# Kernel tuning notes

Measured on AMD Instinct MI355X. Metric: run time of the kernel, lower is better.

Reference implementation:

```python
import jax, jax.numpy as jnp
import numpy as np

DIM = 256
NUM_HEADS = 4
HEAD_DIM = DIM // NUM_HEADS


def setup_inputs() -> dict:
    key = jax.random.key(0)
    ks = jax.random.split(key, 8)
    B, N, C = 4, 2048, DIM
    x = jax.random.normal(ks[0], (B, N, C), dtype=jnp.float32)
    R = jax.random.normal(ks[1], (B, 3, 3), dtype=jnp.float32)
    P = jax.random.normal(ks[2], (N, 3), dtype=jnp.float32)
    s = 1.0 / np.sqrt(C)
    qkv_w = jax.random.normal(ks[3], (3 * C, C), dtype=jnp.float32) * s
    qkv_b = jax.random.normal(ks[4], (3 * C,), dtype=jnp.float32) * 0.02
    proj_w = jax.random.normal(ks[5], (C, C), dtype=jnp.float32) * s
    proj_b = jax.random.normal(ks[6], (C,), dtype=jnp.float32) * 0.02
    pos_scale = jnp.asarray(1.0, dtype=jnp.float32)
    return {"x": x, "R": R, "P": P, "qkv_w": qkv_w, "qkv_b": qkv_b,
            "proj_w": proj_w, "proj_b": proj_b, "pos_scale": pos_scale}


def reference(x, R, P, qkv_w, qkv_b, proj_w, proj_b, pos_scale):
    B, N, C = x.shape
    H, D = NUM_HEADS, HEAD_DIM
    scale = D ** -0.5
    # qkv: (B,N,3C) -> (3,B,H,N,D)
    qkv = (x @ qkv_w.T + qkv_b).reshape(B, N, 3, H, D).transpose(2, 0, 3, 1, 4)
    q, k, v = qkv[0], qkv[1], qkv[2]
    # attention logits (B,H,N,N)
    attn = jnp.einsum('bhid,bhjd->bhij', q, k) * scale
    # positional bias: RP = (R @ P^T)^T -> (B,N,3); bias_ij = dot(RP_i, P_j)
    RP = jnp.einsum('bab,jb->bja', R, P) if False else jnp.einsum('bca,ja->bjc', jnp.swapaxes(R, 1, 2), P)
    RP = jnp.einsum('bcd,jd->bjc', R, P)  # (B,N,3): (R @ P.T).T
    bias = jnp.einsum('bik,jk->bij', RP, P)[:, None, :, :] * pos_scale  # (B,1,N,N) broadcast over heads
    attn = jax.nn.softmax(attn + bias, axis=-1)
    out = jnp.einsum('bhij,bhjd->bhid', attn, v)  # (B,H,N,D)
    out = out.transpose(0, 2, 1, 3).reshape(B, N, C)
    out = out @ proj_w.T + proj_b
    return out
```

## Files before the change

kernel.cpp:

```cpp
#include <hip/hip_runtime.h>
#include <hip/hip_bf16.h>

#define B_ 4
#define N_ 2048
#define C_ 256
#define H_ 4
#define D_ 64

typedef __attribute__((ext_vector_type(8))) short bf16x8;
typedef __attribute__((ext_vector_type(4))) float f32x4;

#define LOG2E 1.4426950408889634f

static __device__ inline unsigned short f2bf(float f) {
    unsigned u = __builtin_bit_cast(unsigned, f);
    unsigned r = (u + 0x7fffu + ((u >> 16) & 1u)) >> 16;
    return (unsigned short)r;
}
static __device__ inline float bf2f(unsigned short h) {
    unsigned u = ((unsigned)h) << 16;
    return __builtin_bit_cast(float, u);
}
static __device__ inline unsigned pack2(float a, float b) {
    __hip_bfloat162 h = __float22bfloat162_rn(make_float2(a, b));
    unsigned u;
    __builtin_memcpy(&u, &h, 4);
    return u;
}
static __device__ inline bf16x8 ld_frag(const unsigned short* p) {
    return __builtin_bit_cast(bf16x8, *(const uint4*)p);
}
static __device__ inline void gload_lds16(const unsigned short* g, unsigned short* l) {
    __builtin_amdgcn_global_load_lds(
        (const __attribute__((address_space(1))) unsigned int*)(g),
        (__attribute__((address_space(3))) unsigned int*)(l),
        16, 0, 0);
}

__global__ __launch_bounds__(256) void cvt_kernel(
    const float* __restrict__ x, const float* __restrict__ qkv_w,
    const float* __restrict__ proj_w, const float* __restrict__ Pm,
    unsigned short* __restrict__ xb, unsigned short* __restrict__ wqb,
    unsigned short* __restrict__ wpb, unsigned short* __restrict__ eb)
{
    const int bid = blockIdx.x, tid = threadIdx.x;
    if (bid >= 1152) {
        const int n = (bid - 1152) * 256 + tid;
        const float* pp = Pm + n * 3;
        float p0 = pp[0], p1 = pp[1], p2 = pp[2];
        unsigned u0 = f2bf(p0), u1 = f2bf(p1), u2 = f2bf(p2);
        unsigned v0 = f2bf(p0 - bf2f((unsigned short)u0));
        unsigned v1 = f2bf(p1 - bf2f((unsigned short)u1));
        unsigned v2 = f2bf(p2 - bf2f((unsigned short)u2));
        uint4 lo, hi;
        lo.x = u0 | (u1 << 16); lo.y = u2 | (v0 << 16);
        lo.z = v1 | (v2 << 16); lo.w = u0 | (u1 << 16);
        hi.x = u2; hi.y = 0u; hi.z = 0u; hi.w = 0u;
        *(uint4*)&eb[n * 16 + 0] = lo;
        *(uint4*)&eb[n * 16 + 8] = hi;
        return;
    }
    const float* s; unsigned short* d; int i;
    if (bid < 1024)      { s = x;      d = xb;  i = (bid * 256 + tid) * 8; }
    else if (bid < 1120) { s = qkv_w;  d = wqb; i = ((bid - 1024) * 256 + tid) * 8; }
    else                 { s = proj_w; d = wpb; i = ((bid - 1120) * 256 + tid) * 8; }
    float4 a = *(const float4*)(s + i);
    float4 b = *(const float4*)(s + i + 4);
    uint4 u;
    u.x = pack2(a.x, a.y); u.y = pack2(a.z, a.w);
    u.z = pack2(b.x, b.y); u.w = pack2(b.z, b.w);
    *(uint4*)(d + i) = u;
}

__global__ __launch_bounds__(256) void qkv_gemm(
    const unsigned short* __restrict__ xb, const unsigned short* __restrict__ wb,
    const float* __restrict__ bias, unsigned short* __restrict__ qb,
    unsigned short* __restrict__ kb, unsigned short* __restrict__ vt)
{
    __shared__ __align__(16) unsigned short As[128 * 40];
    __shared__ __align__(16) unsigned short Bs[128 * 40];
    const int m0 = blockIdx.x * 128, o0 = blockIdx.y * 128;
    const int tid = threadIdx.x;
    const int wave = tid >> 6, lane = tid & 63, quad = lane >> 4, l16 = lane & 15;
    const int wy = wave >> 1, wx = wave & 1;

    f32x4 acc[4][4];
    #pragma unroll
    for (int i = 0; i < 4; ++i)
        #pragma unroll
        for (int j = 0; j < 4; ++j) acc[i][j] = (f32x4){0.f, 0.f, 0.f, 0.f};

    const int srow = tid >> 1, soff = (tid & 1) * 16;

    for (int k0 = 0; k0 < 256; k0 += 32) {
        __syncthreads();
        {
            const unsigned short* sa = &xb[(size_t)(m0 + srow) * 256 + k0 + soff];
            const unsigned short* sb = &wb[(size_t)(o0 + srow) * 256 + k0 + soff];
            *(uint4*)&As[srow * 40 + soff + 0] = *(const uint4*)(sa + 0);
            *(uint4*)&As[srow * 40 + soff + 8] = *(const uint4*)(sa + 8);
            *(uint4*)&Bs[srow * 40 + soff + 0] = *(const uint4*)(sb + 0);
            *(uint4*)&Bs[srow * 40 + soff + 8] = *(const uint4*)(sb + 8);
        }
        __syncthreads();
        bf16x8 a[4], b[4];
        #pragma unroll
        for (int mt = 0; mt < 4; ++mt) a[mt] = ld_frag(&As[(wy * 64 + mt * 16 + l16) * 40 + quad * 8]);
        #pragma unroll
        for (int nt = 0; nt < 4; ++nt) b[nt] = ld_frag(&Bs[(wx * 64 + nt * 16 + l16) * 40 + quad * 8]);
        #pragma unroll
        for (int mt = 0; mt < 4; ++mt)
            #pragma unroll
            for (int nt = 0; nt < 4; ++nt)
                acc[mt][nt] = __builtin_amdgcn_mfma_f32_16x16x32_bf16(a[mt], b[nt], acc[mt][nt], 0, 0, 0);
    }

    const int sec = o0 + wx * 64;
    const int three = sec >> 8;
    const int h = (sec >> 6) & 3;
    const int b = m0 >> 11;
    float bv[4];
    #pragma unroll
    for (int nt = 0; nt < 4; ++nt) bv[nt] = bias[sec + nt * 16 + l16];

    if (three == 2) {
        const int n64 = (m0 + wy * 64) & 2047;
        const size_t bh64 = ((size_t)b * H_ + h) * 64;
        #pragma unroll
        for (int nt = 0; nt < 4; ++nt) {
            int d = nt * 16 + l16;
            #pragma unroll
            for (int r = 0; r < 4; ++r) {
                ushort4 v;
                v.x = f2bf(acc[0][nt][r] + bv[nt]);
                v.y = f2bf(acc[1][nt][r] + bv[nt]);
                v.z = f2bf(acc[2][nt][r] + bv[nt]);
                v.w = f2bf(acc[3][nt][r] + bv[nt]);
                *(ushort4*)&vt[(bh64 + d) * N_ + n64 + 16 * quad + 4 * r] = v;
            }
        }
    } else {
        unsigned short* dst = (three == 0) ? qb : kb;
        float sc = (three == 0) ? (0.125f * LOG2E) : 1.0f;
        #pragma unroll
        for (int mt = 0; mt < 4; ++mt)
            #pragma unroll
            for (int r = 0; r < 4; ++r) {
                int n = (m0 + wy * 64 + mt * 16 + quad * 4 + r) & 2047;
                size_t rowbase = (((size_t)b * H_ + h) * N_ + n) * D_;
                #pragma unroll
                for (int nt = 0; nt < 4; ++nt)
                    dst[rowbase + nt * 16 + l16] = f2bf((acc[mt][nt][r] + bv[nt]) * sc);
            }
    }
}

#define LDK 64

__global__ __launch_bounds__(256) void attn_kernel(
    const unsigned short* __restrict__ qb, const unsigned short* __restrict__ kb,
    const unsigned short* __restrict__ vt, const unsigned short* __restrict__ eb,
    const float* __restrict__ Rm, const float* __restrict__ Pm,
    const float* __restrict__ ps_ptr,
    unsigned short* __restrict__ Opart, float* __restrict__ ml)
{
    __shared__ __align__(16) unsigned short Ks[2][64 * LDK];
    __shared__ __align__(16) unsigned short Vs[2][64 * LDK];
    __shared__ __align__(16) unsigned short Ps[64 * LDK];

    const int bh = blockIdx.y;
    const int b = bh >> 2;
    const int i0 = blockIdx.x * 64;
    const int split = blockIdx.z;
    const int tid = threadIdx.x;
    const int wave = tid >> 6, lane = tid & 63;
    const int quad = lane >> 4, l16 = lane & 15;
    const int x7 = l16 & 7;
    const float ps = ps_ptr[0];

    const size_t base = (size_t)bh * N_ * D_;
    const unsigned short* qg = qb + base;
    const unsigned short* kg = kb + base;
    const unsigned short* vg = vt + base;

    const int jbeg = split * (N_ / 2);
    const int NT = (N_ / 2) / 64;

    const int rl = lane >> 3, sl = lane & 7;
    const int swz = (sl ^ rl) * 8;
    const unsigned short* kq = kg + (size_t)(jbeg + wave * 16 + rl) * D_ + swz;
    const unsigned short* vq = vg + (size_t)(wave * 16 + rl) * N_ + jbeg + swz;
    const unsigned short* ep = eb + (size_t)(jbeg + l16) * 16 + (quad & 1) * 8;

    auto ISSUE = [&](int nb) {
        unsigned short* kd = &Ks[nb][(wave * 16) * LDK];
        unsigned short* vd = &Vs[nb][(wave * 16) * LDK];
        gload_lds16(kq,           kd);
        gload_lds16(kq + 8 * D_,  kd + 8 * LDK);
        gload_lds16(vq,           vd);
        gload_lds16(vq + 8 * N_,  vd + 8 * LDK);
    };

    ISSUE(0);
    kq += 64 * D_; vq += 64;
    bf16x8 ereg[4];
    #pragma unroll
    for (int t = 0; t < 4; ++t) ereg[t] = ld_frag(ep + t * 256);
    ep += 64 * 16;

    const int qrow = i0 + wave * 16 + l16;
    bf16x8 aq[3];
    #pragma unroll
    for (int ks = 0; ks < 2; ++ks)
        aq[ks] = ld_frag(&qg[(size_t)qrow * D_ + ks * 32 + quad * 8]);

    {
        float p0 = Pm[qrow * 3 + 0], p1 = Pm[qrow * 3 + 1], p2 = Pm[qrow * 3 + 2];
        float sc = ps * LOG2E;
        unsigned short ah[3], al[3];
        #pragma unroll
        for (int c = 0; c < 3; ++c) {
            float a = (Rm[b * 9 + c * 3 + 0] * p0 + Rm[b * 9 + c * 3 + 1] * p1
                     + Rm[b * 9 + c * 3 + 2] * p2) * sc;
            ah[c] = f2bf(a);
            al[c] = f2bf(a - bf2f(ah[c]));
        }
        bf16x8 e = (bf16x8){0,0,0,0,0,0,0,0};
        if (quad == 0) {
            e[0] = (short)ah[0]; e[1] = (short)ah[1]; e[2] = (short)ah[2];
            e[3] = (short)ah[0]; e[4] = (short)ah[1]; e[5] = (short)ah[2];
            e[6] = (short)al[0]; e[7] = (short)al[1];
        } else if (quad == 1) {
            e[0] = (short)al[2];
        }
        aq[2] = e;
    }

    const bf16x8 ones = (bf16x8){0x3F80,0x3F80,0x3F80,0x3F80,0x3F80,0x3F80,0x3F80,0x3F80};

    float m_run = -1e30f;
    f32x4 o_acc[4], lacc;
    #pragma unroll
    for (int t = 0; t < 4; ++t) o_acc[t] = (f32x4){0.f, 0.f, 0.f, 0.f};
    lacc = (f32x4){0.f, 0.f, 0.f, 0.f};

    for (int jt = 0; jt < NT; ++jt) {
        const int cur = jt & 1;
        asm volatile("s_waitcnt vmcnt(0)" ::: "memory");
        __syncthreads();
        if (jt + 1 < NT) {
            ISSUE(cur ^ 1);
            kq += 64 * D_; vq += 64;
        }

        f32x4 s[4];
        __builtin_amdgcn_s_setprio(1);
        #pragma unroll
        for (int t = 0; t < 4; ++t) {
            const int rb = (l16 + 16 * t) * LDK;
            f32x4 c = {0.f, 0.f, 0.f, 0.f};
            #pragma unroll
            for (int ks = 0; ks < 2; ++ks) {
                bf16x8 bk = ld_frag(&Ks[cur][rb + (((ks * 4 + quad) ^ x7) * 8)]);
                c = __builtin_amdgcn_mfma_f32_16x16x32_bf16(aq[ks], bk, c, 0, 0, 0);
            }
            c = __builtin_amdgcn_mfma_f32_16x16x32_bf16(aq[2], ereg[t], c, 0, 0, 0);
            s[t] = c;
        }
        __builtin_amdgcn_s_setprio(0);

        if (jt + 1 < NT) {
            #pragma unroll
            for (int t = 0; t < 4; ++t) ereg[t] = ld_frag(ep + t * 256);
            ep += 64 * 16;
        }

        float mx = s[0][0];
        #pragma unroll
        for (int t = 0; t < 4; ++t)
            #pragma unroll
            for (int r = 0; r < 4; ++r)
                mx = fmaxf(mx, s[t][r]);
        #pragma unroll
        for (int off = 1; off < 16; off <<= 1)
            mx = fmaxf(mx, __shfl_xor(mx, off));

        if (__any(mx > m_run + 8.0f)) {
            float mnew = fmaxf(m_run, mx);
            float alpha = exp2f(m_run - mnew);
            #pragma unroll
            for (int t = 0; t < 4; ++t)
                #pragma unroll
                for (int r = 0; r < 4; ++r)
                    o_acc[t][r] *= alpha;
            #pragma unroll
            for (int r = 0; r < 4; ++r) lacc[r] *= alpha;
            m_run = mnew;
        }

        #pragma unroll
        for (int r = 0; r < 4; ++r) {
            float p0 = exp2f(s[0][r] - m_run), p1 = exp2f(s[1][r] - m_run);
            float p2 = exp2f(s[2][r] - m_run), p3 = exp2f(s[3][r] - m_run);
            uint2 w;
            w.x = pack2(p0, p1);
            w.y = pack2(p2, p3);
            const int prow = quad * 4 + r;
            *(uint2*)&Ps[(wave * 16 + prow) * LDK
                         + (((l16 >> 1) ^ (prow & 7)) * 8) + (l16 & 1) * 4] = w;
        }

        __builtin_amdgcn_s_setprio(1);
        #pragma unroll
        for (int ks = 0; ks < 2; ++ks) {
            bf16x8 ap = ld_frag(&Ps[(wave * 16 + l16) * LDK
                                    + (((ks * 4 + quad) ^ x7) * 8)]);
            #pragma unroll
            for (int t = 0; t < 4; ++t) {
                bf16x8 bv = ld_frag(&Vs[cur][(l16 + 16 * t) * LDK
                                             + (((ks * 4 + quad) ^ x7) * 8)]);
                o_acc[t] = __builtin_amdgcn_mfma_f32_16x16x32_bf16(ap, bv, o_acc[t], 0, 0, 0);
            }
            lacc = __builtin_amdgcn_mfma_f32_16x16x32_bf16(ap, ones, lacc, 0, 0, 0);
        }
        __builtin_amdgcn_s_setprio(0);
    }

    const size_t pbase = (size_t)(split * 16 + bh) * N_;
    #pragma unroll
    for (int r = 0; r < 4; ++r) {
        int row = i0 + wave * 16 + quad * 4 + r;
        #pragma unroll
        for (int t = 0; t < 4; ++t)
            Opart[(pbase + row) * D_ + l16 + 16 * t] = f2bf(o_acc[t][r]);
        if (l16 == 0) {
            float2* mlp = (float2*)ml;
            mlp[pbase + row] = make_float2(m_run, lacc[r]);
        }
    }
}

__global__ __launch_bounds__(256) void proj_gemm(
    const unsigned short* __restrict__ Opart, const float* __restrict__ ml,
    const unsigned short* __restrict__ wb, const float* __restrict__ bias,
    float* __restrict__ out)
{
    __shared__ __align__(16) unsigned short As[64 * 40];
    __shared__ __align__(16) unsigned short Bs[64 * 40];
    const int m0 = blockIdx.x * 64, o0 = blockIdx.y * 64;
    const int tid = threadIdx.x;
    const int wave = tid >> 6, lane = tid & 63, quad = lane >> 4, l16 = lane & 15;
    const float2* mlp = (const float2*)ml;

    const int srow = tid >> 2, scb = (tid & 3) * 8;
    const int sm = m0 + srow, sb = sm >> 11, sn = sm & 2047;

    float w1h[4], w2h[4];
    #pragma unroll
    for (int h = 0; h < 4; ++h) {
        size_t r1 = (size_t)(sb * 4 + h) * N_ + sn;
        float2 ml1 = mlp[r1], ml2 = mlp[r1 + 16 * N_];
        float mm = fmaxf(ml1.x, ml2.x);
        float w1 = exp2f(ml1.x - mm), w2 = exp2f(ml2.x - mm);
        float inv = 1.f / (ml1.y * w1 + ml2.y * w2);
        w1h[h] = w1 * inv; w2h[h] = w2 * inv;
    }

    f32x4 acc[4];
    #pragma unroll
    for (int j = 0; j < 4; ++j) acc[j] = (f32x4){0.f, 0.f, 0.f, 0.f};

    for (int k0 = 0; k0 < 256; k0 += 32) {
        const int h = k0 >> 6;
        const int d0 = (k0 & 63) + scb;
        __syncthreads();
        {
            size_t r1 = (size_t)(sb * 4 + h) * N_ + sn;
            union { uint4 u; unsigned short s[8]; } a1, a2;
            a1.u = *(const uint4*)&Opart[r1 * D_ + d0];
            a2.u = *(const uint4*)&Opart[(r1 + 16 * N_) * D_ + d0];
            float w1 = w1h[h], w2 = w2h[h];
            uint4 mv;
            unsigned* mp = (unsigned*)&mv;
            #pragma unroll
            for (int j = 0; j < 4; ++j)
                mp[j] = pack2(bf2f(a1.s[2*j]) * w1 + bf2f(a2.s[2*j]) * w2,
                              bf2f(a1.s[2*j+1]) * w1 + bf2f(a2.s[2*j+1]) * w2);
            *(uint4*)&As[srow * 40 + scb] = mv;
            *(uint4*)&Bs[srow * 40 + scb] = *(const uint4*)&wb[(size_t)(o0 + srow) * 256 + k0 + scb];
        }
        __syncthreads();
        bf16x8 a = ld_frag(&As[(wave * 16 + l16) * 40 + quad * 8]);
        #pragma unroll
        for (int nt = 0; nt < 4; ++nt) {
            bf16x8 b = ld_frag(&Bs[(nt * 16 + l16) * 40 + quad * 8]);
            acc[nt] = __builtin_amdgcn_mfma_f32_16x16x32_bf16(a, b, acc[nt], 0, 0, 0);
        }
    }

    float bv[4];
    #pragma unroll
    for (int nt = 0; nt < 4; ++nt) bv[nt] = bias[o0 + nt * 16 + l16];
    #pragma unroll
    for (int r = 0; r < 4; ++r) {
        int m = m0 + wave * 16 + quad * 4 + r;
        #pragma unroll
        for (int nt = 0; nt < 4; ++nt)
            out[(size_t)m * 256 + o0 + nt * 16 + l16] = acc[nt][r] + bv[nt];
    }
}

extern "C" void kernel_launch(void* const* d_in, const int* in_sizes, int n_in,
                              void* d_out, int out_size, void* d_ws, size_t ws_size,
                              hipStream_t stream) {
    const float* x       = (const float*)d_in[0];
    const float* Rm      = (const float*)d_in[1];
    const float* Pm      = (const float*)d_in[2];
    const float* qkv_w   = (const float*)d_in[3];
    const float* qkv_b   = (const float*)d_in[4];
    const float* proj_w  = (const float*)d_in[5];
    const float* proj_b  = (const float*)d_in[6];
    const float* pos_scl = (const float*)d_in[7];
    float* out = (float*)d_out;

    const size_t NE = (size_t)B_ * H_ * N_ * D_;
    unsigned short* xb    = (unsigned short*)d_ws;
    unsigned short* wqb   = xb   + NE;
    unsigned short* wpb   = wqb  + 768 * 256;
    unsigned short* qb    = wpb  + 256 * 256;
    unsigned short* kb    = qb   + NE;
    unsigned short* vtb   = kb   + NE;
    unsigned short* opart = vtb  + NE;
    float*          mlb   = (float*)(opart + 2 * NE);
    unsigned short* eb    = (unsigned short*)(mlb + 2 * 16 * N_ * 2);

    cvt_kernel<<<1160, 256, 0, stream>>>(x, qkv_w, proj_w, Pm, xb, wqb, wpb, eb);
    qkv_gemm<<<dim3(64, 6), 256, 0, stream>>>(xb, wqb, qkv_b, qb, kb, vtb);
    attn_kernel<<<dim3(32, 16, 2), 256, 0, stream>>>(qb, kb, vtb, eb, Rm, Pm, pos_scl, opart, mlb);
    proj_gemm<<<dim3(128, 4), 256, 0, stream>>>(opart, mlb, wpb, proj_b, out);
}
```

Measured before the change: 145.2 us.

## Fuse fp32-to-bf16 conversion into GEMM loads and use DPP row max

Removes the standalone conversion kernel. The QKV and projection GEMMs now read fp32 x and weights directly and pack them to bf16 while staging into LDS, and the P expansion moves into the first few QKV GEMM blocks. This saves a kernel launch and a full write and read of bf16 copies of x and the weights. The cost is twice the global bytes per tile load and re-converting weights in every block. Separately, the attention row-max reduction swaps shfl_xor for DPP row operations.

Result: no change. 144.5 us (-0.5%).

```diff
diff --git a/kernel.cpp b/kernel.cpp
--- a/kernel.cpp
+++ b/kernel.cpp
@@ -36,16 +36,28 @@
         (__attribute__((address_space(3))) unsigned int*)(l),
         16, 0, 0);
 }
-
-__global__ __launch_bounds__(256) void cvt_kernel(
-    const float* __restrict__ x, const float* __restrict__ qkv_w,
-    const float* __restrict__ proj_w, const float* __restrict__ Pm,
-    unsigned short* __restrict__ xb, unsigned short* __restrict__ wqb,
-    unsigned short* __restrict__ wpb, unsigned short* __restrict__ eb)
+template<int CTRL>
+static __device__ inline float fmax_dpp(float x) {
+    int yi = __builtin_amdgcn_update_dpp(0, __builtin_bit_cast(int, x),
+                                         CTRL, 0xf, 0xf, true);
+    return fmaxf(x, __builtin_bit_cast(float, yi));
+}
+
+__global__ __launch_bounds__(256) void qkv_gemm(
+    const float* __restrict__ x, const float* __restrict__ qw,
+    const float* __restrict__ bias, const float* __restrict__ Pm,
+    unsigned short* __restrict__ qb, unsigned short* __restrict__ kb,
+    unsigned short* __restrict__ vt, unsigned short* __restrict__ eb)
 {
-    const int bid = blockIdx.x, tid = threadIdx.x;
-    if (bid >= 1152) {
-        const int n = (bid - 1152) * 256 + tid;
+    __shared__ __align__(16) unsigned short As[128 * 40];
+    __shared__ __align__(16) unsigned short Bs[128 * 40];
+    const int m0 = blockIdx.x * 128, o0 = blockIdx.y * 128;
+    const int tid = threadIdx.x;
+    const int wave = tid >> 6, lane = tid & 63, quad = lane >> 4, l16 = lane & 15;
+    const int wy = wave >> 1, wx = wave & 1;
+
+    if (blockIdx.y == 0 && blockIdx.x < 8) {
+        const int n = blockIdx.x * 256 + tid;
         const float* pp = Pm + n * 3;
         float p0 = pp[0], p1 = pp[1], p2 = pp[2];
         unsigned u0 = f2bf(p0), u1 = f2bf(p1), u2 = f2bf(p2);
@@ -58,31 +70,7 @@
         hi.x = u2; hi.y = 0u; hi.z = 0u; hi.w = 0u;
         *(uint4*)&eb[n * 16 + 0] = lo;
         *(uint4*)&eb[n * 16 + 8] = hi;
-        return;
-    }
-    const float* s; unsigned short* d; int i;
-    if (bid < 1024)      { s = x;      d = xb;  i = (bid * 256 + tid) * 8; }
-    else if (bid < 1120) { s = qkv_w;  d = wqb; i = ((bid - 1024) * 256 + tid) * 8; }
-    else                 { s = proj_w; d = wpb; i = ((bid - 1120) * 256 + tid) * 8; }
-    float4 a = *(const float4*)(s + i);
-    float4 b = *(const float4*)(s + i + 4);
-    uint4 u;
-    u.x = pack2(a.x, a.y); u.y = pack2(a.z, a.w);
-    u.z = pack2(b.x, b.y); u.w = pack2(b.z, b.w);
-    *(uint4*)(d + i) = u;
-}
-
-__global__ __launch_bounds__(256) void qkv_gemm(
-    const unsigned short* __restrict__ xb, const unsigned short* __restrict__ wb,
-    const float* __restrict__ bias, unsigned short* __restrict__ qb,
-    unsigned short* __restrict__ kb, unsigned short* __restrict__ vt)
-{
-    __shared__ __align__(16) unsigned short As[128 * 40];
-    __shared__ __align__(16) unsigned short Bs[128 * 40];
-    const int m0 = blockIdx.x * 128, o0 = blockIdx.y * 128;
-    const int tid = threadIdx.x;
-    const int wave = tid >> 6, lane = tid & 63, quad = lane >> 4, l16 = lane & 15;
-    const int wy = wave >> 1, wx = wave & 1;
+    }
 
     f32x4 acc[4][4];
     #pragma unroll
@@ -95,12 +83,25 @@
     for (int k0 = 0; k0 < 256; k0 += 32) {
         __syncthreads();
         {
-            const unsigned short* sa = &xb[(size_t)(m0 + srow) * 256 + k0 + soff];
-            const unsigned short* sb = &wb[(size_t)(o0 + srow) * 256 + k0 + soff];
-            *(uint4*)&As[srow * 40 + soff + 0] = *(const uint4*)(sa + 0);
-            *(uint4*)&As[srow * 40 + soff + 8] = *(const uint4*)(sa + 8);
-            *(uint4*)&Bs[srow * 40 + soff + 0] = *(const uint4*)(sb + 0);
-            *(uint4*)&Bs[srow * 40 + soff + 8] = *(const uint4*)(sb + 8);
+            const float* sa = &x [(size_t)(m0 + srow) * 256 + k0 + soff];
+            const float* sw = &qw[(size_t)(o0 + srow) * 256 + k0 + soff];
+            float4 a0 = *(const float4*)(sa + 0),  a1 = *(const float4*)(sa + 4);
+            float4 a2 = *(const float4*)(sa + 8),  a3 = *(const float4*)(sa + 12);
+            float4 b0 = *(const float4*)(sw + 0),  b1 = *(const float4*)(sw + 4);
+            float4 b2 = *(const float4*)(sw + 8),  b3 = *(const float4*)(sw + 12);
+            uint4 ua, ub;
+            ua.x = pack2(a0.x, a0.y); ua.y = pack2(a0.z, a0.w);
+            ua.z = pack2(a1.x, a1.y); ua.w = pack2(a1.z, a1.w);
+            *(uint4*)&As[srow * 40 + soff + 0] = ua;
+            ua.x = pack2(a2.x, a2.y); ua.y = pack2(a2.z, a2.w);
+            ua.z = pack2(a3.x, a3.y); ua.w = pack2(a3.z, a3.w);
+            *(uint4*)&As[srow * 40 + soff + 8] = ua;
+            ub.x = pack2(b0.x, b0.y); ub.y = pack2(b0.z, b0.w);
+            ub.z = pack2(b1.x, b1.y); ub.w = pack2(b1.z, b1.w);
+            *(uint4*)&Bs[srow * 40 + soff + 0] = ub;
+            ub.x = pack2(b2.x, b2.y); ub.y = pack2(b2.z, b2.w);
+            ub.z = pack2(b3.x, b3.y); ub.w = pack2(b3.z, b3.w);
+            *(uint4*)&Bs[srow * 40 + soff + 8] = ub;
         }
         __syncthreads();
         bf16x8 a[4], b[4];
@@ -275,15 +276,15 @@
             ep += 64 * 16;
         }
 
-        float mx = s[0][0];
+        float mt[4];
         #pragma unroll
         for (int t = 0; t < 4; ++t)
-            #pragma unroll
-            for (int r = 0; r < 4; ++r)
-                mx = fmaxf(mx, s[t][r]);
-        #pragma unroll
-        for (int off = 1; off < 16; off <<= 1)
-            mx = fmaxf(mx, __shfl_xor(mx, off));
+            mt[t] = fmaxf(fmaxf(s[t][0], s[t][1]), fmaxf(s[t][2], s[t][3]));
+        float mx = fmaxf(fmaxf(mt[0], mt[1]), fmaxf(mt[2], mt[3]));
+        mx = fmax_dpp<0xB1>(mx);
+        mx = fmax_dpp<0x4E>(mx);
+        mx = fmax_dpp<0x124>(mx);
+        mx = fmax_dpp<0x128>(mx);
 
         if (__any(mx > m_run + 8.0f)) {
             float mnew = fmaxf(m_run, mx);
@@ -342,7 +343,7 @@
 
 __global__ __launch_bounds__(256) void proj_gemm(
     const unsigned short* __restrict__ Opart, const float* __restrict__ ml,
-    const unsigned short* __restrict__ wb, const float* __restrict__ bias,
+    const float* __restrict__ pw, const float* __restrict__ bias,
     float* __restrict__ out)
 {
     __shared__ __align__(16) unsigned short As[64 * 40];
@@ -387,7 +388,12 @@
                 mp[j] = pack2(bf2f(a1.s[2*j]) * w1 + bf2f(a2.s[2*j]) * w2,
                               bf2f(a1.s[2*j+1]) * w1 + bf2f(a2.s[2*j+1]) * w2);
             *(uint4*)&As[srow * 40 + scb] = mv;
-            *(uint4*)&Bs[srow * 40 + scb] = *(const uint4*)&wb[(size_t)(o0 + srow) * 256 + k0 + scb];
+            const float* sw = &pw[(size_t)(o0 + srow) * 256 + k0 + scb];
+            float4 b0 = *(const float4*)(sw + 0), b1 = *(const float4*)(sw + 4);
+            uint4 ub;
+            ub.x = pack2(b0.x, b0.y); ub.y = pack2(b0.z, b0.w);
+            ub.z = pack2(b1.x, b1.y); ub.w = pack2(b1.z, b1.w);
+            *(uint4*)&Bs[srow * 40 + scb] = ub;
         }
         __syncthreads();
         bf16x8 a = ld_frag(&As[(wave * 16 + l16) * 40 + quad * 8]);
@@ -424,18 +430,14 @@
     float* out = (float*)d_out;
 
     const size_t NE = (size_t)B_ * H_ * N_ * D_;
-    unsigned short* xb    = (unsigned short*)d_ws;
-    unsigned short* wqb   = xb   + NE;
-    unsigned short* wpb   = wqb  + 768 * 256;
-    unsigned short* qb    = wpb  + 256 * 256;
+    unsigned short* qb    = (unsigned short*)d_ws;
     unsigned short* kb    = qb   + NE;
     unsigned short* vtb   = kb   + NE;
     unsigned short* opart = vtb  + NE;
     float*          mlb   = (float*)(opart + 2 * NE);
     unsigned short* eb    = (unsigned short*)(mlb + 2 * 16 * N_ * 2);
 
-    cvt_kernel<<<1160, 256, 0, stream>>>(x, qkv_w, proj_w, Pm, xb, wqb, wpb, eb);
-    qkv_gemm<<<dim3(64, 6), 256, 0, stream>>>(xb, wqb, qkv_b, qb, kb, vtb);
+    qkv_gemm<<<dim3(64, 6), 256, 0, stream>>>(x, qkv_w, qkv_b, Pm, qb, kb, vtb, eb);
     attn_kernel<<<dim3(32, 16, 2), 256, 0, stream>>>(qb, kb, vtb, eb, Rm, Pm, pos_scl, opart, mlb);
-    proj_gemm<<<dim3(128, 4), 256, 0, stream>>>(opart, mlb, wpb, proj_b, out);
-}
+    proj_gemm<<<dim3(128, 4), 256, 0, stream>>>(opart, mlb, proj_w, proj_b, out);
+}
```

## Split attention KV range four ways and restructure K/V prefetch pipeline

Applied to the files above, without the earlier changes.

Raises the flash-attention KV split from 2 to 4, doubling the grid to 4096 blocks for better CU occupancy, and extends the proj GEMM merge to combine four partial outputs with their max/sum statistics. Inside the loop, V now uses a single LDS buffer loaded at the start of each tile and waited on (vmcnt) with an extra barrier before the PV MFMAs. K stays double-buffered and the positional-bias fragments are prefetched one tile ahead. The row-max reduction replaces shfl_xor with DPP fmax ops. The cost is more partial-output traffic and merge work, plus an extra barrier per tile. The workspace is reordered so xb aliases the larger opart buffer.

Result: no change. 143.8 us (-1.0%).

```diff
diff --git a/kernel.cpp b/kernel.cpp
--- a/kernel.cpp
+++ b/kernel.cpp
@@ -35,6 +35,12 @@
         (const __attribute__((address_space(1))) unsigned int*)(g),
         (__attribute__((address_space(3))) unsigned int*)(l),
         16, 0, 0);
+}
+template<int CTRL>
+static __device__ inline float fmax_dpp(float x) {
+    int yi = __builtin_amdgcn_update_dpp(0, __builtin_bit_cast(int, x),
+                                         CTRL, 0xf, 0xf, true);
+    return fmaxf(x, __builtin_bit_cast(float, yi));
 }
 
 __global__ __launch_bounds__(256) void cvt_kernel(
@@ -165,7 +171,7 @@
     unsigned short* __restrict__ Opart, float* __restrict__ ml)
 {
     __shared__ __align__(16) unsigned short Ks[2][64 * LDK];
-    __shared__ __align__(16) unsigned short Vs[2][64 * LDK];
+    __shared__ __align__(16) unsigned short Vs[64 * LDK];
     __shared__ __align__(16) unsigned short Ps[64 * LDK];
 
     const int bh = blockIdx.y;
@@ -183,8 +189,8 @@
     const unsigned short* kg = kb + base;
     const unsigned short* vg = vt + base;
 
-    const int jbeg = split * (N_ / 2);
-    const int NT = (N_ / 2) / 64;
+    const int jbeg = split * (N_ / 4);
+    const int NT = (N_ / 4) / 64;
 
     const int rl = lane >> 3, sl = lane & 7;
     const int swz = (sl ^ rl) * 8;
@@ -192,17 +198,12 @@
     const unsigned short* vq = vg + (size_t)(wave * 16 + rl) * N_ + jbeg + swz;
     const unsigned short* ep = eb + (size_t)(jbeg + l16) * 16 + (quad & 1) * 8;
 
-    auto ISSUE = [&](int nb) {
-        unsigned short* kd = &Ks[nb][(wave * 16) * LDK];
-        unsigned short* vd = &Vs[nb][(wave * 16) * LDK];
-        gload_lds16(kq,           kd);
-        gload_lds16(kq + 8 * D_,  kd + 8 * LDK);
-        gload_lds16(vq,           vd);
-        gload_lds16(vq + 8 * N_,  vd + 8 * LDK);
-    };
-
-    ISSUE(0);
-    kq += 64 * D_; vq += 64;
+    {
+        unsigned short* kd = &Ks[0][(wave * 16) * LDK];
+        gload_lds16(kq,          kd);
+        gload_lds16(kq + 8 * D_, kd + 8 * LDK);
+        kq += 64 * D_;
+    }
     bf16x8 ereg[4];
     #pragma unroll
     for (int t = 0; t < 4; ++t) ereg[t] = ld_frag(ep + t * 256);
@@ -246,12 +247,31 @@
 
     for (int jt = 0; jt < NT; ++jt) {
         const int cur = jt & 1;
+        const bool more = (jt + 1 < NT);
+
         asm volatile("s_waitcnt vmcnt(0)" ::: "memory");
-        __syncthreads();
-        if (jt + 1 < NT) {
-            ISSUE(cur ^ 1);
-            kq += 64 * D_; vq += 64;
-        }
+        __builtin_amdgcn_s_barrier();
+        __builtin_amdgcn_sched_barrier(0);
+
+        bf16x8 enext[4];
+        if (more) {
+            #pragma unroll
+            for (int t = 0; t < 4; ++t) enext[t] = ld_frag(ep + t * 256);
+            ep += 64 * 16;
+        }
+        {
+            unsigned short* vd = &Vs[(wave * 16) * LDK];
+            gload_lds16(vq,          vd);
+            gload_lds16(vq + 8 * N_, vd + 8 * LDK);
+            vq += 64;
+        }
+        if (more) {
+            unsigned short* kd = &Ks[cur ^ 1][(wave * 16) * LDK];
+            gload_lds16(kq,          kd);
+            gload_lds16(kq + 8 * D_, kd + 8 * LDK);
+            kq += 64 * D_;
+        }
+        __builtin_amdgcn_sched_barrier(0);
 
         f32x4 s[4];
         __builtin_amdgcn_s_setprio(1);
@@ -268,22 +288,20 @@
             s[t] = c;
         }
         __builtin_amdgcn_s_setprio(0);
-
-        if (jt + 1 < NT) {
-            #pragma unroll
-            for (int t = 0; t < 4; ++t) ereg[t] = ld_frag(ep + t * 256);
-            ep += 64 * 16;
-        }
-
-        float mx = s[0][0];
+        if (more) {
+            #pragma unroll
+            for (int t = 0; t < 4; ++t) ereg[t] = enext[t];
+        }
+
+        float mt[4];
         #pragma unroll
         for (int t = 0; t < 4; ++t)
-            #pragma unroll
-            for (int r = 0; r < 4; ++r)
-                mx = fmaxf(mx, s[t][r]);
-        #pragma unroll
-        for (int off = 1; off < 16; off <<= 1)
-            mx = fmaxf(mx, __shfl_xor(mx, off));
+            mt[t] = fmaxf(fmaxf(s[t][0], s[t][1]), fmaxf(s[t][2], s[t][3]));
+        float mx = fmaxf(fmaxf(mt[0], mt[1]), fmaxf(mt[2], mt[3]));
+        mx = fmax_dpp<0xB1>(mx);
+        mx = fmax_dpp<0x4E>(mx);
+        mx = fmax_dpp<0x124>(mx);
+        mx = fmax_dpp<0x128>(mx);
 
         if (__any(mx > m_run + 8.0f)) {
             float mnew = fmaxf(m_run, mx);
@@ -310,6 +328,11 @@
                          + (((l16 >> 1) ^ (prow & 7)) * 8) + (l16 & 1) * 4] = w;
         }
 
+        if (more) asm volatile("s_waitcnt vmcnt(2)" ::: "memory");
+        else      asm volatile("s_waitcnt vmcnt(0)" ::: "memory");
+        __builtin_amdgcn_s_barrier();
+        __builtin_amdgcn_sched_barrier(0);
+
         __builtin_amdgcn_s_setprio(1);
         #pragma unroll
         for (int ks = 0; ks < 2; ++ks) {
@@ -317,8 +340,8 @@
                                     + (((ks * 4 + quad) ^ x7) * 8)]);
             #pragma unroll
             for (int t = 0; t < 4; ++t) {
-                bf16x8 bv = ld_frag(&Vs[cur][(l16 + 16 * t) * LDK
-                                             + (((ks * 4 + quad) ^ x7) * 8)]);
+                bf16x8 bv = ld_frag(&Vs[(l16 + 16 * t) * LDK
+                                        + (((ks * 4 + quad) ^ x7) * 8)]);
                 o_acc[t] = __builtin_amdgcn_mfma_f32_16x16x32_bf16(ap, bv, o_acc[t], 0, 0, 0);
             }
             lacc = __builtin_amdgcn_mfma_f32_16x16x32_bf16(ap, ones, lacc, 0, 0, 0);
@@ -355,15 +378,18 @@
     const int srow = tid >> 2, scb = (tid & 3) * 8;
     const int sm = m0 + srow, sb = sm >> 11, sn = sm & 2047;
 
-    float w1h[4], w2h[4];
+    float wgt[4][4];
     #pragma unroll
     for (int h = 0; h < 4; ++h) {
         size_t r1 = (size_t)(sb * 4 + h) * N_ + sn;
-        float2 ml1 = mlp[r1], ml2 = mlp[r1 + 16 * N_];
-        float mm = fmaxf(ml1.x, ml2.x);
-        float w1 = exp2f(ml1.x - mm), w2 = exp2f(ml2.x - mm);
-        float inv = 1.f / (ml1.y * w1 + ml2.y * w2);
-        w1h[h] = w1 * inv; w2h[h] = w2 * inv;
+        float2 m0v = mlp[r1], m1v = mlp[r1 + 16 * N_];
+        float2 m2v = mlp[r1 + 32 * N_], m3v = mlp[r1 + 48 * N_];
+        float mm = fmaxf(fmaxf(m0v.x, m1v.x), fmaxf(m2v.x, m3v.x));
+        float w0 = exp2f(m0v.x - mm), w1 = exp2f(m1v.x - mm);
+        float w2 = exp2f(m2v.x - mm), w3 = exp2f(m3v.x - mm);
+        float inv = 1.f / (m0v.y * w0 + m1v.y * w1 + m2v.y * w2 + m3v.y * w3);
+        wgt[h][0] = w0 * inv; wgt[h][1] = w1 * inv;
+        wgt[h][2] = w2 * inv; wgt[h][3] = w3 * inv;
     }
 
     f32x4 acc[4];
@@ -376,16 +402,22 @@
         __syncthreads();
         {
             size_t r1 = (size_t)(sb * 4 + h) * N_ + sn;
-            union { uint4 u; unsigned short s[8]; } a1, a2;
-            a1.u = *(const uint4*)&Opart[r1 * D_ + d0];
-            a2.u = *(const uint4*)&Opart[(r1 + 16 * N_) * D_ + d0];
-            float w1 = w1h[h], w2 = w2h[h];
+            union { uint4 u; unsigned short s[8]; } a0, a1, a2, a3;
+            a0.u = *(const uint4*)&Opart[(r1 +  0 * N_) * D_ + d0];
+            a1.u = *(const uint4*)&Opart[(r1 + 16 * N_) * D_ + d0];
+            a2.u = *(const uint4*)&Opart[(r1 + 32 * N_) * D_ + d0];
+            a3.u = *(const uint4*)&Opart[(r1 + 48 * N_) * D_ + d0];
+            float w0 = wgt[h][0], w1 = wgt[h][1], w2 = wgt[h][2], w3 = wgt[h][3];
             uint4 mv;
             unsigned* mp = (unsigned*)&mv;
             #pragma unroll
-            for (int j = 0; j < 4; ++j)
-                mp[j] = pack2(bf2f(a1.s[2*j]) * w1 + bf2f(a2.s[2*j]) * w2,
-                              bf2f(a1.s[2*j+1]) * w1 + bf2f(a2.s[2*j+1]) * w2);
+            for (int j = 0; j < 4; ++j) {
+                float lo = bf2f(a0.s[2*j]) * w0 + bf2f(a1.s[2*j]) * w1
+                         + bf2f(a2.s[2*j]) * w2 + bf2f(a3.s[2*j]) * w3;
+                float hi = bf2f(a0.s[2*j+1]) * w0 + bf2f(a1.s[2*j+1]) * w1
+                         + bf2f(a2.s[2*j+1]) * w2 + bf2f(a3.s[2*j+1]) * w3;
+                mp[j] = pack2(lo, hi);
+            }
             *(uint4*)&As[srow * 40 + scb] = mv;
             *(uint4*)&Bs[srow * 40 + scb] = *(const uint4*)&wb[(size_t)(o0 + srow) * 256 + k0 + scb];
         }
@@ -424,18 +456,18 @@
     float* out = (float*)d_out;
 
     const size_t NE = (size_t)B_ * H_ * N_ * D_;
-    unsigned short* xb    = (unsigned short*)d_ws;
-    unsigned short* wqb   = xb   + NE;
-    unsigned short* wpb   = wqb  + 768 * 256;
-    unsigned short* qb    = wpb  + 256 * 256;
+    unsigned short* opart = (unsigned short*)d_ws;
+    unsigned short* qb    = opart + 4 * NE;
     unsigned short* kb    = qb   + NE;
     unsigned short* vtb   = kb   + NE;
-    unsigned short* opart = vtb  + NE;
-    float*          mlb   = (float*)(opart + 2 * NE);
-    unsigned short* eb    = (unsigned short*)(mlb + 2 * 16 * N_ * 2);
+    float*          mlb   = (float*)(vtb + NE);
+    unsigned short* eb    = (unsigned short*)(mlb + (size_t)4 * 16 * N_ * 2);
+    unsigned short* wqb   = eb  + 2048 * 16;
+    unsigned short* wpb   = wqb + 768 * 256;
+    unsigned short* xb    = opart;
 
     cvt_kernel<<<1160, 256, 0, stream>>>(x, qkv_w, proj_w, Pm, xb, wqb, wpb, eb);
     qkv_gemm<<<dim3(64, 6), 256, 0, stream>>>(xb, wqb, qkv_b, qb, kb, vtb);
-    attn_kernel<<<dim3(32, 16, 2), 256, 0, stream>>>(qb, kb, vtb, eb, Rm, Pm, pos_scl, opart, mlb);
+    attn_kernel<<<dim3(32, 16, 4), 256, 0, stream>>>(qb, kb, vtb, eb, Rm, Pm, pos_scl, opart, mlb);
     proj_gemm<<<dim3(128, 4), 256, 0, stream>>>(opart, mlb, wpb, proj_b, out);
 }
```
